# Optimization experiments

Measured on AMD Instinct MI355X. Metric: run time of the kernel, lower is better.

Reference implementation:

```python
import jax, jax.numpy as jnp
import numpy as np

DT = 1e-3
TAU_SYN_INV = 50.0   # overridden in SeqNet.__init__
TAU_MEM_INV = 100.0  # norse default
V_TH = 1.0
EPS = 1e-5
H1 = 512
H2 = 512
NOUT = 10


def setup_inputs() -> dict:
    key = jax.random.key(0)
    ks = jax.random.split(key, 11)
    T, B, F = 100, 512, 784
    x = jax.random.normal(ks[0], (T, B, F), dtype=jnp.float32)
    # torch.nn.Linear init ~ U(-1/sqrt(fan_in), 1/sqrt(fan_in))
    def lin(k, out_d, in_d):
        bound = 1.0 / np.sqrt(in_d)
        kw, kb = jax.random.split(k)
        W = jax.random.uniform(kw, (out_d, in_d), jnp.float32, -bound, bound)
        b = jax.random.uniform(kb, (out_d,), jnp.float32, -bound, bound)
        return W, b
    W0, b0 = lin(ks[1], H1, F)
    W1, b1 = lin(ks[2], H2, H1)
    g0 = jnp.ones((H1,), jnp.float32)
    bt0 = jnp.zeros((H1,), jnp.float32)
    g1 = jnp.ones((H2,), jnp.float32)
    bt1 = jnp.zeros((H2,), jnp.float32)
    # norse LILinearCell: input_weights ~ randn / sqrt(hidden), no bias
    Wo = jax.random.normal(ks[3], (NOUT, H2), jnp.float32) / np.sqrt(H2)
    return {"x": x, "W0": W0, "b0": b0, "W1": W1, "b1": b1,
            "g0": g0, "bt0": bt0, "g1": g1, "bt1": bt1, "Wo": Wo}


def _bn(z, g, b):
    # BatchNorm1d in training mode: per-step batch statistics (biased var)
    m = jnp.mean(z, axis=0)
    v = jnp.var(z, axis=0)
    return g * (z - m) * jax.lax.rsqrt(v + EPS) + b


def _lif_step(v, i, cur):
    # norse lif_feed_forward_step, v_leak=0, v_reset=0
    v_dec = v + DT * TAU_MEM_INV * (-v + i)          # membrane decay + input current
    i_dec = i * (1.0 - DT * TAU_SYN_INV)             # synaptic decay
    z = (v_dec - V_TH > 0).astype(cur.dtype)         # heaviside spike
    v_new = (1.0 - z) * v_dec                        # reset to 0 on spike
    i_new = i_dec + cur                              # inject weighted input
    return z, v_new, i_new


def reference(x, W0, b0, W1, b1, g0, bt0, g1, bt1, Wo):
    T, B = x.shape[0], x.shape[1]
    xf = x.reshape(T, B, -1)

    def step(carry, xt):
        v0, i0, v1, i1, vo, io = carry
        cur0 = xt @ W0.T + b0                        # [B, H1]
        z0, v0, i0 = _lif_step(v0, i0, cur0)
        h0 = _bn(z0, g0, bt0)
        cur1 = h0 @ W1.T + b1                        # [B, H2]
        z1, v1, i1 = _lif_step(v1, i1, cur1)
        h1 = _bn(z1, g1, bt1)
        # norse LILinearCell (li_step): leaky integrator, returns v
        vo_new = vo + DT * TAU_MEM_INV * (-vo + io)  # [B, 10]
        io_new = io * (1.0 - DT * TAU_SYN_INV) + h1 @ Wo.T
        return (v0, i0, v1, i1, vo_new, io_new), vo_new

    z32 = lambda d: jnp.zeros((B, d), x.dtype)
    carry0 = (z32(W0.shape[0]), z32(W0.shape[0]),
              z32(W1.shape[0]), z32(W1.shape[0]),
              z32(Wo.shape[0]), z32(Wo.shape[0]))
    _, voltages = jax.lax.scan(step, carry0, xf)
    return voltages  # [T, B, 10]
```

## Files before the change

kernel.cpp:

```cpp
#include <hip/hip_runtime.h>
#include <stdint.h>

#define T_    100
#define B_    512
#define F_    784
#define FP_   800
#define H_    512
#define NOUT_ 10
#define R_    (T_*B_)
#define BH    (B_*H_)

typedef _Float16 f16x8 __attribute__((ext_vector_type(8)));
typedef float    f32x4 __attribute__((ext_vector_type(4)));

__device__ __forceinline__ void gload_lds16(const void* g, void* l) {
    __builtin_amdgcn_global_load_lds(
        (const __attribute__((address_space(1))) uint32_t*)g,
        (__attribute__((address_space(3))) uint32_t*)l, 16, 0, 0);
}

__global__ void convW_kernel(const float* __restrict__ W, _Float16* __restrict__ Wh,
                             _Float16* __restrict__ Wl, int K, int Kp, int n)
{
    int idx = blockIdx.x * 256 + threadIdx.x;
    if (idx >= n) return;
    int r = idx / Kp, k = idx - r * Kp;
    float v = (k < K) ? W[r * K + k] : 0.f;
    _Float16 h = (_Float16)v;
    Wh[idx] = h;
    Wl[idx] = (_Float16)(v - (float)h);
}

__global__ __launch_bounds__(256, 2) void gemm0_mfma(
    const float* __restrict__ X, const _Float16* __restrict__ Wh,
    const _Float16* __restrict__ Wl, const float* __restrict__ bias,
    float* __restrict__ C)
{
    __shared__ _Float16 L[40960];
    const int tid  = threadIdx.x;
    const int gl   = (blockIdx.x & 7) * 200 + (blockIdx.x >> 3);
    const int r0   = (gl >> 2) * 128;
    const int n0   = (gl & 3) * 128;
    const int lane = tid & 63;
    const int wm = (tid >> 7) & 1, wn = (tid >> 6) & 1;
    const int frow = lane & 15, fgrp = lane >> 4;

    const int brow = tid >> 2;
    const int bcol = (((tid & 3) ^ ((brow >> 1) & 3)) << 3);
    const _Float16* WhB = Wh + (size_t)(n0 + brow) * FP_ + bcol;
    const _Float16* WlB = Wl + (size_t)(n0 + brow) * FP_ + bcol;

    const int arow = tid >> 1, ahalf = tid & 1;
    const float* Xb = X + (size_t)(r0 + arow) * F_ + ahalf * 16;
    const int aoff = arow * 32;
    const int ac0  = (((ahalf * 2)     ^ ((arow >> 1) & 3)) << 3);
    const int ac1  = (((ahalf * 2 + 1) ^ ((arow >> 1) & 3)) << 3);

    f32x4 acc[4][4];
#pragma unroll
    for (int i = 0; i < 4; i++)
#pragma unroll
        for (int j = 0; j < 4; j++) acc[i][j] = f32x4{0.f, 0.f, 0.f, 0.f};

    auto stageB = [&](int sbuf, int kt) {
        _Float16* dh = L + 16384 + sbuf * 8192;
        _Float16* dl = dh + 4096;
        gload_lds16(WhB + kt,            dh + tid * 8);
        gload_lds16(WhB + 64 * FP_ + kt, dh + 2048 + tid * 8);
        gload_lds16(WlB + kt,            dl + tid * 8);
        gload_lds16(WlB + 64 * FP_ + kt, dl + 2048 + tid * 8);
    };
    auto loadA = [&](float4 (&xa)[4], int kt) {
#pragma unroll
        for (int j = 0; j < 4; j++) {
            int c = kt + ahalf * 16 + j * 4;
            xa[j] = (c < F_) ? *(const float4*)(Xb + kt + j * 4)
                             : make_float4(0.f, 0.f, 0.f, 0.f);
        }
    };
    auto writeA = [&](int abuf, const float4 (&xa)[4]) {
        _Float16* dh = L + abuf * 8192;
        _Float16* dl = dh + 4096;
        const float* v = (const float*)xa;
        f16x8 h0, l0, h1, l1;
#pragma unroll
        for (int j = 0; j < 8; j++) {
            _Float16 a = (_Float16)v[j];
            h0[j] = a; l0[j] = (_Float16)(v[j] - (float)a);
            _Float16 b = (_Float16)v[8 + j];
            h1[j] = b; l1[j] = (_Float16)(v[8 + j] - (float)b);
        }
        *(f16x8*)(dh + aoff + ac0) = h0;
        *(f16x8*)(dh + aoff + ac1) = h1;
        *(f16x8*)(dl + aoff + ac0) = l0;
        *(f16x8*)(dl + aoff + ac1) = l1;
    };

    float4 R0[4], R1[4];
    stageB(0, 0);
    stageB(1, 32);
    loadA(R0, 0);
    loadA(R1, 32);
    writeA(0, R0);
    asm volatile("s_waitcnt lgkmcnt(0)" ::: "memory");
    __builtin_amdgcn_sched_barrier(0);
    __builtin_amdgcn_s_barrier();
    __builtin_amdgcn_sched_barrier(0);

    auto body = [&](int k, int rbuf, int sbuf, float4 (&Rl)[4], float4 (&Rw)[4],
                    bool pf, bool dw) {
        if (pf) { stageB(sbuf, (k + 2) * 32); loadA(Rl, (k + 2) * 32); }
        const _Float16* Ab = L + (k & 1) * 8192;
        const _Float16* Bb = L + 16384 + rbuf * 8192;
        f16x8 ah[4], al[4], bh[4], bl[4];
#pragma unroll
        for (int mi = 0; mi < 4; mi++) {
            int row = wm * 64 + mi * 16 + frow;
            int off = row * 32 + ((fgrp ^ ((row >> 1) & 3)) << 3);
            ah[mi] = *(const f16x8*)(Ab + off);
            al[mi] = *(const f16x8*)(Ab + 4096 + off);
        }
#pragma unroll
        for (int ni = 0; ni < 4; ni++) {
            int row = wn * 64 + ni * 16 + frow;
            int off = row * 32 + ((fgrp ^ ((row >> 1) & 3)) << 3);
            bh[ni] = *(const f16x8*)(Bb + off);
            bl[ni] = *(const f16x8*)(Bb + 4096 + off);
        }
        __builtin_amdgcn_s_setprio(1);
#pragma unroll
        for (int mi = 0; mi < 4; mi++)
#pragma unroll
            for (int ni = 0; ni < 4; ni++) {
                acc[mi][ni] = __builtin_amdgcn_mfma_f32_16x16x32_f16(ah[mi], bh[ni], acc[mi][ni], 0, 0, 0);
                acc[mi][ni] = __builtin_amdgcn_mfma_f32_16x16x32_f16(ah[mi], bl[ni], acc[mi][ni], 0, 0, 0);
                acc[mi][ni] = __builtin_amdgcn_mfma_f32_16x16x32_f16(al[mi], bh[ni], acc[mi][ni], 0, 0, 0);
            }
        __builtin_amdgcn_s_setprio(0);
        if (dw) writeA((k + 1) & 1, Rw);
        asm volatile("s_waitcnt vmcnt(8)" ::: "memory");
        asm volatile("s_waitcnt lgkmcnt(0)" ::: "memory");
        __builtin_amdgcn_sched_barrier(0);
        __builtin_amdgcn_s_barrier();
        __builtin_amdgcn_sched_barrier(0);
    };

    int rb = 0;
    for (int kp = 0; kp < 12; kp++) {
        int k = kp * 2;
        body(k,     rb, rb == 0 ? 2 : rb - 1, R0, R1, (k + 2) <= 24, true);
        rb = (rb == 2) ? 0 : rb + 1;
        body(k + 1, rb, rb == 0 ? 2 : rb - 1, R1, R0, (k + 3) <= 24, true);
        rb = (rb == 2) ? 0 : rb + 1;
    }
    body(24, rb, 0, R0, R1, false, false);

#pragma unroll
    for (int ni = 0; ni < 4; ni++) {
        int col = n0 + wn * 64 + ni * 16 + frow;
        float bv = bias[col];
#pragma unroll
        for (int mi = 0; mi < 4; mi++) {
            int rbase = r0 + wm * 64 + mi * 16 + fgrp * 4;
#pragma unroll
            for (int p = 0; p < 4; p++)
                C[(size_t)(rbase + p) * H_ + col] = acc[mi][ni][p] + bv;
        }
    }
}

__global__ __launch_bounds__(256, 2) void gemm1_mfma(
    const _Float16* __restrict__ Zh, const float* __restrict__ W1,
    const float* __restrict__ alpha, const float* __restrict__ bW,
    float* __restrict__ C)
{
    __shared__ _Float16 L[28672];
    const int tid  = threadIdx.x;
    const int gl   = (blockIdx.x & 7) * 200 + (blockIdx.x >> 3);
    const int r0   = (gl >> 2) * 128;
    const int n0   = (gl & 3) * 128;
    const int tt   = r0 >> 9;
    const int lane = tid & 63;
    const int wm = (tid >> 7) & 1, wn = (tid >> 6) & 1;
    const int frow = lane & 15, fgrp = lane >> 4;

    const int arow = tid >> 2;
    const int acol = (((tid & 3) ^ ((arow >> 1) & 3)) << 3);
    const _Float16* ZhB = Zh + (size_t)(r0 + arow) * H_ + acol;

    const int brow = tid >> 1, bhalf = tid & 1;
    const float* W1B = W1 + (size_t)(n0 + brow) * H_ + bhalf * 16;
    const float* alB = alpha + tt * H_ + bhalf * 16;
    const int boff = brow * 32;
    const int bc0  = (((bhalf * 2)     ^ ((brow >> 1) & 3)) << 3);
    const int bc1  = (((bhalf * 2 + 1) ^ ((brow >> 1) & 3)) << 3);

    f32x4 acc[4][4];
#pragma unroll
    for (int i = 0; i < 4; i++)
#pragma unroll
        for (int j = 0; j < 4; j++) acc[i][j] = f32x4{0.f, 0.f, 0.f, 0.f};

    auto stageA = [&](int sbuf, int kt) {
        _Float16* d = L + sbuf * 4096;
        gload_lds16(ZhB + kt,           d + tid * 8);
        gload_lds16(ZhB + 64 * H_ + kt, d + 2048 + tid * 8);
    };
    auto loadB = [&](float4 (&wv)[4], float4 (&av)[4], int kt) {
#pragma unroll
        for (int j = 0; j < 4; j++) {
            wv[j] = *(const float4*)(W1B + kt + j * 4);
            av[j] = *(const float4*)(alB + kt + j * 4);
        }
    };
    auto writeB = [&](int wbuf, const float4 (&wv)[4], const float4 (&av)[4]) {
        _Float16* dh = L + 12288 + wbuf * 8192;
        _Float16* dl = dh + 4096;
        const float* w = (const float*)wv;
        const float* a = (const float*)av;
        f16x8 h0, l0, h1, l1;
#pragma unroll
        for (int j = 0; j < 8; j++) {
            float p0 = a[j] * w[j];
            _Float16 q0 = (_Float16)p0;
            h0[j] = q0; l0[j] = (_Float16)(p0 - (float)q0);
            float p1 = a[8 + j] * w[8 + j];
            _Float16 q1 = (_Float16)p1;
            h1[j] = q1; l1[j] = (_Float16)(p1 - (float)q1);
        }
        *(f16x8*)(dh + boff + bc0) = h0;
        *(f16x8*)(dh + boff + bc1) = h1;
        *(f16x8*)(dl + boff + bc0) = l0;
        *(f16x8*)(dl + boff + bc1) = l1;
    };

    float4 Wv0[4], Av0[4], Wv1[4], Av1[4];
    stageA(0, 0);
    stageA(1, 32);
    loadB(Wv0, Av0, 0);
    loadB(Wv1, Av1, 32);
    writeB(0, Wv0, Av0);
    asm volatile("s_waitcnt lgkmcnt(0)" ::: "memory");
    __builtin_amdgcn_sched_barrier(0);
    __builtin_amdgcn_s_barrier();
    __builtin_amdgcn_sched_barrier(0);

    auto body = [&](int k, int rbuf, int sbuf, float4 (&Wl_)[4], float4 (&Al_)[4],
                    float4 (&Ww_)[4], float4 (&Aw_)[4], bool pf, bool dw) {
        if (pf) { stageA(sbuf, (k + 2) * 32); loadB(Wl_, Al_, (k + 2) * 32); }
        const _Float16* Ab = L + rbuf * 4096;
        const _Float16* Bb = L + 12288 + (k & 1) * 8192;
        f16x8 az[4], bh[4], bl[4];
#pragma unroll
        for (int mi = 0; mi < 4; mi++) {
            int row = wm * 64 + mi * 16 + frow;
            int off = row * 32 + ((fgrp ^ ((row >> 1) & 3)) << 3);
            az[mi] = *(const f16x8*)(Ab + off);
        }
#pragma unroll
        for (int ni = 0; ni < 4; ni++) {
            int row = wn * 64 + ni * 16 + frow;
            int off = row * 32 + ((fgrp ^ ((row >> 1) & 3)) << 3);
            bh[ni] = *(const f16x8*)(Bb + off);
            bl[ni] = *(const f16x8*)(Bb + 4096 + off);
        }
        __builtin_amdgcn_s_setprio(1);
#pragma unroll
        for (int mi = 0; mi < 4; mi++)
#pragma unroll
            for (int ni = 0; ni < 4; ni++) {
                acc[mi][ni] = __builtin_amdgcn_mfma_f32_16x16x32_f16(az[mi], bh[ni], acc[mi][ni], 0, 0, 0);
                acc[mi][ni] = __builtin_amdgcn_mfma_f32_16x16x32_f16(az[mi], bl[ni], acc[mi][ni], 0, 0, 0);
            }
        __builtin_amdgcn_s_setprio(0);
        if (dw) writeB((k + 1) & 1, Ww_, Aw_);
        asm volatile("s_waitcnt vmcnt(10)" ::: "memory");
        asm volatile("s_waitcnt lgkmcnt(0)" ::: "memory");
        __builtin_amdgcn_sched_barrier(0);
        __builtin_amdgcn_s_barrier();
        __builtin_amdgcn_sched_barrier(0);
    };

    int rb = 0;
    for (int kp = 0; kp < 7; kp++) {
        int k = kp * 2;
        body(k,     rb, rb == 0 ? 2 : rb - 1, Wv0, Av0, Wv1, Av1, true, true);
        rb = (rb == 2) ? 0 : rb + 1;
        body(k + 1, rb, rb == 0 ? 2 : rb - 1, Wv1, Av1, Wv0, Av0, (k + 3) <= 15, true);
        rb = (rb == 2) ? 0 : rb + 1;
    }
    body(14, rb, 0, Wv0, Av0, Wv1, Av1, false, true);
    rb = 0;
    body(15, rb, 0, Wv1, Av1, Wv0, Av0, false, false);

#pragma unroll
    for (int ni = 0; ni < 4; ni++) {
        int col = n0 + wn * 64 + ni * 16 + frow;
        float bv = bW[tt * H_ + col];
#pragma unroll
        for (int mi = 0; mi < 4; mi++) {
            int rbase = r0 + wm * 64 + mi * 16 + fgrp * 4;
#pragma unroll
            for (int p = 0; p < 4; p++)
                C[(size_t)(rbase + p) * H_ + col] = acc[mi][ni][p] + bv;
        }
    }
}

__global__ __launch_bounds__(512) void bw_kernel(
    const float* __restrict__ beta, const float* __restrict__ W1,
    const float* __restrict__ b1, float* __restrict__ bW)
{
    __shared__ float bs[512];
    const int t = blockIdx.x, n = threadIdx.x;
    bs[n] = beta[t * H_ + n];
    __syncthreads();
    const float* wr = W1 + (size_t)n * H_;
    float s = b1[n];
    for (int f = 0; f < H_; f += 4) {
        float4 w = *(const float4*)(wr + f);
        s = fmaf(bs[f],     w.x, s);
        s = fmaf(bs[f + 1], w.y, s);
        s = fmaf(bs[f + 2], w.z, s);
        s = fmaf(bs[f + 3], w.w, s);
    }
    bW[t * H_ + n] = s;
}

__global__ __launch_bounds__(256) void lif_kernel(
    const float* __restrict__ cur, _Float16* __restrict__ z)
{
    const int tid = blockIdx.x * 256 + threadIdx.x;
    float v = 0.f, ii = 0.f;
    const float* p = cur + tid;
    _Float16* q = z + tid;
    for (int t = 0; t < T_; t++) {
        float vd = __fadd_rn(v, __fmul_rn(0.1f, __fsub_rn(ii, v)));
        float id = __fmul_rn(ii, 0.95f);
        int zz = (vd > 1.0f) ? 1 : 0;
        v  = zz ? 0.f : vd;
        ii = __fadd_rn(id, p[(size_t)t * BH]);
        q[(size_t)t * BH] = (_Float16)zz;
    }
}

__global__ __launch_bounds__(512) void bn_part(const _Float16* __restrict__ z,
                                               float* __restrict__ part)
{
    const int t = blockIdx.x >> 3, c = blockIdx.x & 7, h = threadIdx.x;
    const _Float16* p = z + (size_t)t * BH + (size_t)(c * 64) * H_ + h;
    float fs = 0.f;
    for (int b = 0; b < 64; b++) fs += (float)p[(size_t)b * H_];
    part[(size_t)blockIdx.x * H_ + h] = fs;
}

__global__ __launch_bounds__(512) void bn_fin(const float* __restrict__ part,
                          const float* __restrict__ g, const float* __restrict__ bt,
                          float* __restrict__ alpha, float* __restrict__ beta)
{
    const int t = blockIdx.x, h = threadIdx.x;
    float fs = 0.f;
#pragma unroll
    for (int c = 0; c < 8; c++) fs += part[(size_t)(t * 8 + c) * H_ + h];
    float m   = fs * (1.0f / 512.0f);
    float var = __fsub_rn(m, __fmul_rn(m, m));
    float al  = g[h] / sqrtf(__fadd_rn(var, 1e-5f));
    float be  = __fsub_rn(bt[h], __fmul_rn(m, al));
    alpha[t * H_ + h] = al;
    beta [t * H_ + h] = be;
}

__global__ __launch_bounds__(256) void ugemm_kernel(
    const _Float16* __restrict__ Z, const float* __restrict__ alpha,
    const float* __restrict__ beta, const float* __restrict__ Wo,
    float* __restrict__ U)
{
    const int tid  = threadIdx.x;
    const int wave = tid >> 6, lane = tid & 63;
    const size_t r = (size_t)blockIdx.x * 4 + wave;
    const int t = (int)(r >> 9);
    const _Float16* zr = Z + r * 512;
    const float* alp = alpha + t * 512;
    const float* bet = beta  + t * 512;
    float acc[NOUT_];
#pragma unroll
    for (int o = 0; o < NOUT_; o++) acc[o] = 0.f;
#pragma unroll
    for (int jj = 0; jj < 8; jj++) {
        int j = jj * 64 + lane;
        float h = fmaf((float)zr[j], alp[j], bet[j]);
#pragma unroll
        for (int o = 0; o < NOUT_; o++) acc[o] = fmaf(h, Wo[o * 512 + j], acc[o]);
    }
#pragma unroll
    for (int o = 0; o < NOUT_; o++) {
        float v = acc[o];
#pragma unroll
        for (int off = 32; off; off >>= 1) v += __shfl_down(v, off, 64);
        if (lane == 0) U[r * NOUT_ + o] = v;
    }
}

__global__ void li_kernel(const float* __restrict__ U, float* __restrict__ out)
{
    const int tid = blockIdx.x * 256 + threadIdx.x;
    if (tid >= B_ * NOUT_) return;
    float vo = 0.f, io = 0.f;
    for (int t = 0; t < T_; t++) {
        vo = __fadd_rn(vo, __fmul_rn(0.1f, __fsub_rn(io, vo)));
        out[t * (B_ * NOUT_) + tid] = vo;
        io = __fadd_rn(__fmul_rn(io, 0.95f), U[t * (B_ * NOUT_) + tid]);
    }
}

extern "C" void kernel_launch(void* const* d_in, const int* in_sizes, int n_in,
                              void* d_out, int out_size, void* d_ws, size_t ws_size,
                              hipStream_t stream)
{
    const float* X   = (const float*)d_in[0];
    const float* W0  = (const float*)d_in[1];
    const float* b0  = (const float*)d_in[2];
    const float* W1  = (const float*)d_in[3];
    const float* b1  = (const float*)d_in[4];
    const float* g0  = (const float*)d_in[5];
    const float* bt0 = (const float*)d_in[6];
    const float* g1  = (const float*)d_in[7];
    const float* bt1 = (const float*)d_in[8];
    const float* Wo  = (const float*)d_in[9];
    float* out = (float*)d_out;

    char* w = (char*)d_ws;
    float*    CUR    = (float*)w;
    _Float16* Zh     = (_Float16*)(w + 104857600);
    float*    alpha0 = (float*)(w + 104857600 + 52428800);
    float*    beta0  = alpha0 + T_*H_;
    float*    alpha1 = beta0  + T_*H_;
    float*    beta1  = alpha1 + T_*H_;
    float*    bW     = beta1  + T_*H_;
    float*    U      = bW     + T_*H_;
    _Float16* W0h    = (_Float16*)(U + R_*NOUT_);
    _Float16* W0l    = W0h + 512*FP_;
    float*    part   = (float*)(W0l + 512*FP_);

    convW_kernel<<<(512*FP_+255)/256, 256, 0, stream>>>(W0, W0h, W0l, F_, FP_, 512*FP_);

    gemm0_mfma  <<<1600,  256, 0, stream>>>(X, W0h, W0l, b0, CUR);
    lif_kernel  <<<1024,  256, 0, stream>>>(CUR, Zh);
    bn_part     <<<800,   512, 0, stream>>>(Zh, part);
    bn_fin      <<<100,   512, 0, stream>>>(part, g0, bt0, alpha0, beta0);
    bw_kernel   <<<100,   512, 0, stream>>>(beta0, W1, b1, bW);
    gemm1_mfma  <<<1600,  256, 0, stream>>>(Zh, W1, alpha0, bW, CUR);
    lif_kernel  <<<1024,  256, 0, stream>>>(CUR, Zh);
    bn_part     <<<800,   512, 0, stream>>>(Zh, part);
    bn_fin      <<<100,   512, 0, stream>>>(part, g1, bt1, alpha1, beta1);
    ugemm_kernel<<<12800, 256, 0, stream>>>(Zh, alpha1, beta1, Wo, U);
    li_kernel   <<<20,    256, 0, stream>>>(U, out);
}
```

Before: 590.7 us.

## Pre-split X and alpha-folded W1 into fp16 hi/lo buffers for direct-to-LDS GEMMs

A new pre-pass converts X into padded fp16 hi/lo arrays so gemm0 can stage both operands with direct global-to-LDS loads instead of register loads, conversion and LDS writes inside the main loop. A second pre-pass folds the per-timestep BN scale alpha into W1 and splits it into hi/lo fp16 per timestep, so gemm1 also becomes a plain double-buffered async-load GEMM with launch bounds raised to 3 blocks. The cost is extra kernels and much more global traffic: the X conversion writes about 160 MB, and the folded W1 needs around 100 MB of workspace. The old path is kept as a fallback for when the workspace is too small.

```diff
diff --git a/kernel.cpp b/kernel.cpp
--- a/kernel.cpp
+++ b/kernel.cpp
@@ -31,7 +31,244 @@
     Wl[idx] = (_Float16)(v - (float)h);
 }
 
+__global__ __launch_bounds__(256) void convX_kernel(
+    const float* __restrict__ X, _Float16* __restrict__ Xh, _Float16* __restrict__ Xl)
+{
+    int idx = blockIdx.x * 256 + threadIdx.x;
+    if (idx >= R_ * 100) return;
+    int r = idx / 100, c8 = (idx - r * 100) * 8;
+    f16x8 h, l;
+    if (c8 + 8 <= F_) {
+        float4 v0 = *(const float4*)(X + (size_t)r * F_ + c8);
+        float4 v1 = *(const float4*)(X + (size_t)r * F_ + c8 + 4);
+        float v[8] = {v0.x, v0.y, v0.z, v0.w, v1.x, v1.y, v1.z, v1.w};
+#pragma unroll
+        for (int j = 0; j < 8; j++) {
+            _Float16 a = (_Float16)v[j];
+            h[j] = a; l[j] = (_Float16)(v[j] - (float)a);
+        }
+    } else {
+#pragma unroll
+        for (int j = 0; j < 8; j++) { h[j] = (_Float16)0.f; l[j] = (_Float16)0.f; }
+    }
+    *(f16x8*)(Xh + (size_t)r * FP_ + c8) = h;
+    *(f16x8*)(Xl + (size_t)r * FP_ + c8) = l;
+}
+
+__global__ __launch_bounds__(256) void foldW1_kernel(
+    const float* __restrict__ W1, const float* __restrict__ alpha,
+    _Float16* __restrict__ Wfh, _Float16* __restrict__ Wfl)
+{
+    int idx = blockIdx.x * 256 + threadIdx.x;
+    if (idx >= 100 * 512 * 64) return;
+    int t = idx >> 15, rem = idx & 32767, n = rem >> 6, f8 = (rem & 63) * 8;
+    float4 w0 = *(const float4*)(W1 + (size_t)n * H_ + f8);
+    float4 w1 = *(const float4*)(W1 + (size_t)n * H_ + f8 + 4);
+    float4 a0 = *(const float4*)(alpha + t * H_ + f8);
+    float4 a1 = *(const float4*)(alpha + t * H_ + f8 + 4);
+    float w[8] = {w0.x, w0.y, w0.z, w0.w, w1.x, w1.y, w1.z, w1.w};
+    float a[8] = {a0.x, a0.y, a0.z, a0.w, a1.x, a1.y, a1.z, a1.w};
+    f16x8 h, l;
+#pragma unroll
+    for (int j = 0; j < 8; j++) {
+        float p = a[j] * w[j];
+        _Float16 q = (_Float16)p;
+        h[j] = q; l[j] = (_Float16)(p - (float)q);
+    }
+    size_t o = ((size_t)t * H_ + n) * H_ + f8;
+    *(f16x8*)(Wfh + o) = h;
+    *(f16x8*)(Wfl + o) = l;
+}
+
 __global__ __launch_bounds__(256, 2) void gemm0_mfma(
+    const _Float16* __restrict__ Xh, const _Float16* __restrict__ Xl,
+    const _Float16* __restrict__ Wh, const _Float16* __restrict__ Wl,
+    const float* __restrict__ bias, float* __restrict__ C)
+{
+    __shared__ _Float16 L[2 * 16384];
+    const int tid  = threadIdx.x;
+    const int gl   = (blockIdx.x & 7) * 200 + (blockIdx.x >> 3);
+    const int r0   = (gl >> 2) * 128;
+    const int n0   = (gl & 3) * 128;
+    const int lane = tid & 63;
+    const int wm = (tid >> 7) & 1, wn = (tid >> 6) & 1;
+    const int frow = lane & 15, fgrp = lane >> 4;
+
+    const int drow = tid >> 2;
+    const int dcol = (((tid & 3) ^ ((drow >> 1) & 3)) << 3);
+    const _Float16* XhB = Xh + (size_t)(r0 + drow) * FP_ + dcol;
+    const _Float16* XlB = Xl + (size_t)(r0 + drow) * FP_ + dcol;
+    const _Float16* WhB = Wh + (size_t)(n0 + drow) * FP_ + dcol;
+    const _Float16* WlB = Wl + (size_t)(n0 + drow) * FP_ + dcol;
+
+    f32x4 acc[4][4];
+#pragma unroll
+    for (int i = 0; i < 4; i++)
+#pragma unroll
+        for (int j = 0; j < 4; j++) acc[i][j] = f32x4{0.f, 0.f, 0.f, 0.f};
+
+    auto stage = [&](int buf, int kt) {
+        _Float16* b = L + buf * 16384;
+        gload_lds16(XhB + kt,            b + tid * 8);
+        gload_lds16(XhB + 64 * FP_ + kt, b + 2048 + tid * 8);
+        gload_lds16(XlB + kt,            b + 4096 + tid * 8);
+        gload_lds16(XlB + 64 * FP_ + kt, b + 6144 + tid * 8);
+        gload_lds16(WhB + kt,            b + 8192 + tid * 8);
+        gload_lds16(WhB + 64 * FP_ + kt, b + 10240 + tid * 8);
+        gload_lds16(WlB + kt,            b + 12288 + tid * 8);
+        gload_lds16(WlB + 64 * FP_ + kt, b + 14336 + tid * 8);
+    };
+
+    stage(0, 0);
+    for (int k = 0; k < 25; k++) {
+        if (k < 24) {
+            stage((k + 1) & 1, (k + 1) * 32);
+            asm volatile("s_waitcnt vmcnt(8)" ::: "memory");
+        } else {
+            asm volatile("s_waitcnt vmcnt(0)" ::: "memory");
+        }
+        __builtin_amdgcn_sched_barrier(0);
+        __builtin_amdgcn_s_barrier();
+        __builtin_amdgcn_sched_barrier(0);
+
+        const _Float16* bp = L + (k & 1) * 16384;
+        f16x8 ah[4], al[4], bh[4], bl[4];
+#pragma unroll
+        for (int mi = 0; mi < 4; mi++) {
+            int row = wm * 64 + mi * 16 + frow;
+            int off = row * 32 + ((fgrp ^ ((row >> 1) & 3)) << 3);
+            ah[mi] = *(const f16x8*)(bp + off);
+            al[mi] = *(const f16x8*)(bp + 4096 + off);
+        }
+#pragma unroll
+        for (int ni = 0; ni < 4; ni++) {
+            int row = wn * 64 + ni * 16 + frow;
+            int off = row * 32 + ((fgrp ^ ((row >> 1) & 3)) << 3);
+            bh[ni] = *(const f16x8*)(bp + 8192 + off);
+            bl[ni] = *(const f16x8*)(bp + 12288 + off);
+        }
+        __builtin_amdgcn_s_setprio(1);
+#pragma unroll
+        for (int mi = 0; mi < 4; mi++)
+#pragma unroll
+            for (int ni = 0; ni < 4; ni++) {
+                acc[mi][ni] = __builtin_amdgcn_mfma_f32_16x16x32_f16(ah[mi], bh[ni], acc[mi][ni], 0, 0, 0);
+                acc[mi][ni] = __builtin_amdgcn_mfma_f32_16x16x32_f16(ah[mi], bl[ni], acc[mi][ni], 0, 0, 0);
+                acc[mi][ni] = __builtin_amdgcn_mfma_f32_16x16x32_f16(al[mi], bh[ni], acc[mi][ni], 0, 0, 0);
+            }
+        __builtin_amdgcn_s_setprio(0);
+        __builtin_amdgcn_sched_barrier(0);
+        __builtin_amdgcn_s_barrier();
+        __builtin_amdgcn_sched_barrier(0);
+    }
+
+#pragma unroll
+    for (int ni = 0; ni < 4; ni++) {
+        int col = n0 + wn * 64 + ni * 16 + frow;
+        float bv = bias[col];
+#pragma unroll
+        for (int mi = 0; mi < 4; mi++) {
+            int rbase = r0 + wm * 64 + mi * 16 + fgrp * 4;
+#pragma unroll
+            for (int p = 0; p < 4; p++)
+                C[(size_t)(rbase + p) * H_ + col] = acc[mi][ni][p] + bv;
+        }
+    }
+}
+
+__global__ __launch_bounds__(256, 3) void gemm1_mfma(
+    const _Float16* __restrict__ Zh, const _Float16* __restrict__ Wfh,
+    const _Float16* __restrict__ Wfl, const float* __restrict__ bW,
+    float* __restrict__ C)
+{
+    __shared__ _Float16 L[2 * 12288];
+    const int tid  = threadIdx.x;
+    const int gl   = (blockIdx.x & 7) * 200 + (blockIdx.x >> 3);
+    const int r0   = (gl >> 2) * 128;
+    const int n0   = (gl & 3) * 128;
+    const int tt   = gl >> 4;
+    const int lane = tid & 63;
+    const int wm = (tid >> 7) & 1, wn = (tid >> 6) & 1;
+    const int frow = lane & 15, fgrp = lane >> 4;
+
+    const int drow = tid >> 2;
+    const int dcol = (((tid & 3) ^ ((drow >> 1) & 3)) << 3);
+    const _Float16* ZhB = Zh + (size_t)(r0 + drow) * H_ + dcol;
+    const _Float16* WfhB = Wfh + ((size_t)tt * H_ + n0 + drow) * H_ + dcol;
+    const _Float16* WflB = Wfl + ((size_t)tt * H_ + n0 + drow) * H_ + dcol;
+
+    f32x4 acc[4][4];
+#pragma unroll
+    for (int i = 0; i < 4; i++)
+#pragma unroll
+        for (int j = 0; j < 4; j++) acc[i][j] = f32x4{0.f, 0.f, 0.f, 0.f};
+
+    auto stage = [&](int buf, int kt) {
+        _Float16* b = L + buf * 12288;
+        gload_lds16(ZhB + kt,            b + tid * 8);
+        gload_lds16(ZhB + 64 * H_ + kt,  b + 2048 + tid * 8);
+        gload_lds16(WfhB + kt,           b + 4096 + tid * 8);
+        gload_lds16(WfhB + 64 * H_ + kt, b + 6144 + tid * 8);
+        gload_lds16(WflB + kt,           b + 8192 + tid * 8);
+        gload_lds16(WflB + 64 * H_ + kt, b + 10240 + tid * 8);
+    };
+
+    stage(0, 0);
+    for (int k = 0; k < 16; k++) {
+        if (k < 15) {
+            stage((k + 1) & 1, (k + 1) * 32);
+            asm volatile("s_waitcnt vmcnt(6)" ::: "memory");
+        } else {
+            asm volatile("s_waitcnt vmcnt(0)" ::: "memory");
+        }
+        __builtin_amdgcn_sched_barrier(0);
+        __builtin_amdgcn_s_barrier();
+        __builtin_amdgcn_sched_barrier(0);
+
+        const _Float16* bp = L + (k & 1) * 12288;
+        f16x8 az[4], bh[4], bl[4];
+#pragma unroll
+        for (int mi = 0; mi < 4; mi++) {
+            int row = wm * 64 + mi * 16 + frow;
+            int off = row * 32 + ((fgrp ^ ((row >> 1) & 3)) << 3);
+            az[mi] = *(const f16x8*)(bp + off);
+        }
+#pragma unroll
+        for (int ni = 0; ni < 4; ni++) {
+            int row = wn * 64 + ni * 16 + frow;
+            int off = row * 32 + ((fgrp ^ ((row >> 1) & 3)) << 3);
+            bh[ni] = *(const f16x8*)(bp + 4096 + off);
+            bl[ni] = *(const f16x8*)(bp + 8192 + off);
+        }
+        __builtin_amdgcn_s_setprio(1);
+#pragma unroll
+        for (int mi = 0; mi < 4; mi++)
+#pragma unroll
+            for (int ni = 0; ni < 4; ni++) {
+                acc[mi][ni] = __builtin_amdgcn_mfma_f32_16x16x32_f16(az[mi], bh[ni], acc[mi][ni], 0, 0, 0);
+                acc[mi][ni] = __builtin_amdgcn_mfma_f32_16x16x32_f16(az[mi], bl[ni], acc[mi][ni], 0, 0, 0);
+            }
+        __builtin_amdgcn_s_setprio(0);
+        __builtin_amdgcn_sched_barrier(0);
+        __builtin_amdgcn_s_barrier();
+        __builtin_amdgcn_sched_barrier(0);
+    }
+
+#pragma unroll
+    for (int ni = 0; ni < 4; ni++) {
+        int col = n0 + wn * 64 + ni * 16 + frow;
+        float bv = bW[tt * H_ + col];
+#pragma unroll
+        for (int mi = 0; mi < 4; mi++) {
+            int rbase = r0 + wm * 64 + mi * 16 + fgrp * 4;
+#pragma unroll
+            for (int p = 0; p < 4; p++)
+                C[(size_t)(rbase + p) * H_ + col] = acc[mi][ni][p] + bv;
+        }
+    }
+}
+
+__global__ __launch_bounds__(256, 2) void gemm0_old(
     const float* __restrict__ X, const _Float16* __restrict__ Wh,
     const _Float16* __restrict__ Wl, const float* __restrict__ bias,
     float* __restrict__ C)
@@ -44,24 +281,20 @@
     const int lane = tid & 63;
     const int wm = (tid >> 7) & 1, wn = (tid >> 6) & 1;
     const int frow = lane & 15, fgrp = lane >> 4;
-
     const int brow = tid >> 2;
     const int bcol = (((tid & 3) ^ ((brow >> 1) & 3)) << 3);
     const _Float16* WhB = Wh + (size_t)(n0 + brow) * FP_ + bcol;
     const _Float16* WlB = Wl + (size_t)(n0 + brow) * FP_ + bcol;
-
     const int arow = tid >> 1, ahalf = tid & 1;
     const float* Xb = X + (size_t)(r0 + arow) * F_ + ahalf * 16;
     const int aoff = arow * 32;
     const int ac0  = (((ahalf * 2)     ^ ((arow >> 1) & 3)) << 3);
     const int ac1  = (((ahalf * 2 + 1) ^ ((arow >> 1) & 3)) << 3);
-
     f32x4 acc[4][4];
 #pragma unroll
     for (int i = 0; i < 4; i++)
 #pragma unroll
         for (int j = 0; j < 4; j++) acc[i][j] = f32x4{0.f, 0.f, 0.f, 0.f};
-
     auto stageB = [&](int sbuf, int kt) {
         _Float16* dh = L + 16384 + sbuf * 8192;
         _Float16* dl = dh + 4096;
@@ -95,18 +328,12 @@
         *(f16x8*)(dl + aoff + ac0) = l0;
         *(f16x8*)(dl + aoff + ac1) = l1;
     };
-
     float4 R0[4], R1[4];
-    stageB(0, 0);
-    stageB(1, 32);
-    loadA(R0, 0);
-    loadA(R1, 32);
-    writeA(0, R0);
+    stageB(0, 0); stageB(1, 32); loadA(R0, 0); loadA(R1, 32); writeA(0, R0);
     asm volatile("s_waitcnt lgkmcnt(0)" ::: "memory");
     __builtin_amdgcn_sched_barrier(0);
     __builtin_amdgcn_s_barrier();
     __builtin_amdgcn_sched_barrier(0);
-
     auto body = [&](int k, int rbuf, int sbuf, float4 (&Rl)[4], float4 (&Rw)[4],
                     bool pf, bool dw) {
         if (pf) { stageB(sbuf, (k + 2) * 32); loadA(Rl, (k + 2) * 32); }
@@ -144,7 +371,6 @@
         __builtin_amdgcn_s_barrier();
         __builtin_amdgcn_sched_barrier(0);
     };
-
     int rb = 0;
     for (int kp = 0; kp < 12; kp++) {
         int k = kp * 2;
@@ -154,7 +380,6 @@
         rb = (rb == 2) ? 0 : rb + 1;
     }
     body(24, rb, 0, R0, R1, false, false);
-
 #pragma unroll
     for (int ni = 0; ni < 4; ni++) {
         int col = n0 + wn * 64 + ni * 16 + frow;
@@ -169,7 +394,7 @@
     }
 }
 
-__global__ __launch_bounds__(256, 2) void gemm1_mfma(
+__global__ __launch_bounds__(256, 2) void gemm1_old(
     const _Float16* __restrict__ Zh, const float* __restrict__ W1,
     const float* __restrict__ alpha, const float* __restrict__ bW,
     float* __restrict__ C)
@@ -183,24 +408,20 @@
     const int lane = tid & 63;
     const int wm = (tid >> 7) & 1, wn = (tid >> 6) & 1;
     const int frow = lane & 15, fgrp = lane >> 4;
-
     const int arow = tid >> 2;
     const int acol = (((tid & 3) ^ ((arow >> 1) & 3)) << 3);
     const _Float16* ZhB = Zh + (size_t)(r0 + arow) * H_ + acol;
-
     const int brow = tid >> 1, bhalf = tid & 1;
     const float* W1B = W1 + (size_t)(n0 + brow) * H_ + bhalf * 16;
     const float* alB = alpha + tt * H_ + bhalf * 16;
     const int boff = brow * 32;
     const int bc0  = (((bhalf * 2)     ^ ((brow >> 1) & 3)) << 3);
     const int bc1  = (((bhalf * 2 + 1) ^ ((brow >> 1) & 3)) << 3);
-
     f32x4 acc[4][4];
 #pragma unroll
     for (int i = 0; i < 4; i++)
 #pragma unroll
         for (int j = 0; j < 4; j++) acc[i][j] = f32x4{0.f, 0.f, 0.f, 0.f};
-
     auto stageA = [&](int sbuf, int kt) {
         _Float16* d = L + sbuf * 4096;
         gload_lds16(ZhB + kt,           d + tid * 8);
@@ -233,18 +454,13 @@
         *(f16x8*)(dl + boff + bc0) = l0;
         *(f16x8*)(dl + boff + bc1) = l1;
     };
-
     float4 Wv0[4], Av0[4], Wv1[4], Av1[4];
-    stageA(0, 0);
-    stageA(1, 32);
-    loadB(Wv0, Av0, 0);
-    loadB(Wv1, Av1, 32);
+    stageA(0, 0); stageA(1, 32); loadB(Wv0, Av0, 0); loadB(Wv1, Av1, 32);
     writeB(0, Wv0, Av0);
     asm volatile("s_waitcnt lgkmcnt(0)" ::: "memory");
     __builtin_amdgcn_sched_barrier(0);
     __builtin_amdgcn_s_barrier();
     __builtin_amdgcn_sched_barrier(0);
-
     auto body = [&](int k, int rbuf, int sbuf, float4 (&Wl_)[4], float4 (&Al_)[4],
                     float4 (&Ww_)[4], float4 (&Aw_)[4], bool pf, bool dw) {
         if (pf) { stageA(sbuf, (k + 2) * 32); loadB(Wl_, Al_, (k + 2) * 32); }
@@ -280,7 +496,6 @@
         __builtin_amdgcn_s_barrier();
         __builtin_amdgcn_sched_barrier(0);
     };
-
     int rb = 0;
     for (int kp = 0; kp < 7; kp++) {
         int k = kp * 2;
@@ -292,7 +507,6 @@
     body(14, rb, 0, Wv0, Av0, Wv1, Av1, false, true);
     rb = 0;
     body(15, rb, 0, Wv1, Av1, Wv0, Av0, false, false);
-
 #pragma unroll
     for (int ni = 0; ni < 4; ni++) {
         int col = n0 + wn * 64 + ni * 16 + frow;
@@ -430,29 +644,61 @@
     float* out = (float*)d_out;
 
     char* w = (char*)d_ws;
-    float*    CUR    = (float*)w;
-    _Float16* Zh     = (_Float16*)(w + 104857600);
-    float*    alpha0 = (float*)(w + 104857600 + 52428800);
-    float*    beta0  = alpha0 + T_*H_;
-    float*    alpha1 = beta0  + T_*H_;
-    float*    beta1  = alpha1 + T_*H_;
-    float*    bW     = beta1  + T_*H_;
-    float*    U      = bW     + T_*H_;
-    _Float16* W0h    = (_Float16*)(U + R_*NOUT_);
-    _Float16* W0l    = W0h + 512*FP_;
-    float*    part   = (float*)(W0l + 512*FP_);
-
-    convW_kernel<<<(512*FP_+255)/256, 256, 0, stream>>>(W0, W0h, W0l, F_, FP_, 512*FP_);
-
-    gemm0_mfma  <<<1600,  256, 0, stream>>>(X, W0h, W0l, b0, CUR);
-    lif_kernel  <<<1024,  256, 0, stream>>>(CUR, Zh);
-    bn_part     <<<800,   512, 0, stream>>>(Zh, part);
-    bn_fin      <<<100,   512, 0, stream>>>(part, g0, bt0, alpha0, beta0);
-    bw_kernel   <<<100,   512, 0, stream>>>(beta0, W1, b1, bW);
-    gemm1_mfma  <<<1600,  256, 0, stream>>>(Zh, W1, alpha0, bW, CUR);
-    lif_kernel  <<<1024,  256, 0, stream>>>(CUR, Zh);
-    bn_part     <<<800,   512, 0, stream>>>(Zh, part);
-    bn_fin      <<<100,   512, 0, stream>>>(part, g1, bt1, alpha1, beta1);
-    ugemm_kernel<<<12800, 256, 0, stream>>>(Zh, alpha1, beta1, Wo, U);
-    li_kernel   <<<20,    256, 0, stream>>>(U, out);
-}
+    const size_t NEED = 327475200ull;
+
+    if (ws_size >= NEED) {
+        float*    CUR    = (float*)w;
+        _Float16* Zh     = (_Float16*)(w + 104857600);
+        _Float16* XA     = (_Float16*)(w + 157286400);
+        _Float16* XB     = (_Float16*)(w + 239206400);
+        float*    alpha0 = (float*)(w + 321126400);
+        float*    beta0  = alpha0 + T_*H_;
+        float*    alpha1 = beta0  + T_*H_;
+        float*    beta1  = alpha1 + T_*H_;
+        float*    bW     = beta1  + T_*H_;
+        float*    U      = bW     + T_*H_;
+        _Float16* W0h    = (_Float16*)(U + R_*NOUT_);
+        _Float16* W0l    = W0h + 512*FP_;
+        float*    part   = (float*)(W0l + 512*FP_);
+
+        convX_kernel<<<20000, 256, 0, stream>>>(X, XA, XB);
+        convW_kernel<<<(512*FP_+255)/256, 256, 0, stream>>>(W0, W0h, W0l, F_, FP_, 512*FP_);
+        gemm0_mfma  <<<1600,  256, 0, stream>>>(XA, XB, W0h, W0l, b0, CUR);
+        lif_kernel  <<<1024,  256, 0, stream>>>(CUR, Zh);
+        bn_part     <<<800,   512, 0, stream>>>(Zh, part);
+        bn_fin      <<<100,   512, 0, stream>>>(part, g0, bt0, alpha0, beta0);
+        bw_kernel   <<<100,   512, 0, stream>>>(beta0, W1, b1, bW);
+        foldW1_kernel<<<12800,256, 0, stream>>>(W1, alpha0, XA, XB);
+        gemm1_mfma  <<<1600,  256, 0, stream>>>(Zh, XA, XB, bW, CUR);
+        lif_kernel  <<<1024,  256, 0, stream>>>(CUR, Zh);
+        bn_part     <<<800,   512, 0, stream>>>(Zh, part);
+        bn_fin      <<<100,   512, 0, stream>>>(part, g1, bt1, alpha1, beta1);
+        ugemm_kernel<<<12800, 256, 0, stream>>>(Zh, alpha1, beta1, Wo, U);
+        li_kernel   <<<20,    256, 0, stream>>>(U, out);
+    } else {
+        float*    CUR    = (float*)w;
+        _Float16* Zh     = (_Float16*)(w + 104857600);
+        float*    alpha0 = (float*)(w + 104857600 + 52428800);
+        float*    beta0  = alpha0 + T_*H_;
+        float*    alpha1 = beta0  + T_*H_;
+        float*    beta1  = alpha1 + T_*H_;
+        float*    bW     = beta1  + T_*H_;
+        float*    U      = bW     + T_*H_;
+        _Float16* W0h    = (_Float16*)(U + R_*NOUT_);
+        _Float16* W0l    = W0h + 512*FP_;
+        float*    part   = (float*)(W0l + 512*FP_);
+
+        convW_kernel<<<(512*FP_+255)/256, 256, 0, stream>>>(W0, W0h, W0l, F_, FP_, 512*FP_);
+        gemm0_old   <<<1600,  256, 0, stream>>>(X, W0h, W0l, b0, CUR);
+        lif_kernel  <<<1024,  256, 0, stream>>>(CUR, Zh);
+        bn_part     <<<800,   512, 0, stream>>>(Zh, part);
+        bn_fin      <<<100,   512, 0, stream>>>(part, g0, bt0, alpha0, beta0);
+        bw_kernel   <<<100,   512, 0, stream>>>(beta0, W1, b1, bW);
+        gemm1_old   <<<1600,  256, 0, stream>>>(Zh, W1, alpha0, bW, CUR);
+        lif_kernel  <<<1024,  256, 0, stream>>>(CUR, Zh);
+        bn_part     <<<800,   512, 0, stream>>>(Zh, part);
+        bn_fin      <<<100,   512, 0, stream>>>(part, g1, bt1, alpha1, beta1);
+        ugemm_kernel<<<12800, 256, 0, stream>>>(Zh, alpha1, beta1, Wo, U);
+        li_kernel   <<<20,    256, 0, stream>>>(U, out);
+    }
+}
```

Result: slower. 665.2 us (+12.6%).
